# Kernel tuning notes

Hardware: AMD Instinct MI355X
Metric: run time of the kernel (lower is better)

The kernel has to match this reference:

```python
import jax, jax.numpy as jnp
import numpy as np

N = 50000        # nodes
E = 1_600_000    # edges (avg degree 32)
F_IN = 128       # node feature dim
H = 64           # hidden_channels
C = 19           # output classes
G = 512          # graphs in the batch


def setup_inputs() -> dict:
    key = jax.random.key(0)
    ks = jax.random.split(key, 9)
    x = jax.random.normal(ks[0], (N, F_IN), dtype=jnp.float32)
    edge_index = jax.random.randint(ks[1], (2, E), 0, N, dtype=jnp.int64)
    batch = jnp.sort(jax.random.randint(ks[2], (N,), 0, G, dtype=jnp.int64))
    W1 = jax.random.normal(ks[3], (F_IN, H), dtype=jnp.float32) / np.sqrt(F_IN)
    b1 = jnp.zeros((H,), dtype=jnp.float32)
    W2 = jax.random.normal(ks[4], (H, H), dtype=jnp.float32) / np.sqrt(H)
    b2 = jnp.zeros((H,), dtype=jnp.float32)
    W_out = jax.random.normal(ks[5], (H, C), dtype=jnp.float32) / np.sqrt(H)
    b_out = jnp.zeros((C,), dtype=jnp.float32)
    return {"x": x, "edge_index": edge_index, "batch": batch,
            "W1": W1, "b1": b1, "W2": W2, "b2": b2,
            "W_out": W_out, "b_out": b_out}


def _gcn_conv(x, src, dst, W, b, n_nodes):
    """PyG GCNConv: add self-loops, symmetric D^-1/2 (A+I) D^-1/2 norm,
    linear transform first, gather-scale-scatter aggregation, then bias."""
    x = x @ W  # [N, out]
    loop = jnp.arange(n_nodes, dtype=src.dtype)
    s = jnp.concatenate([src, loop])  # source (message origin)
    d = jnp.concatenate([dst, loop])  # target (aggregation site)
    deg = jax.ops.segment_sum(jnp.ones_like(d, dtype=x.dtype), d,
                              num_segments=n_nodes)
    dinv = jnp.where(deg > 0, jax.lax.rsqrt(deg), 0.0)
    norm = dinv[s] * dinv[d]                       # [E+N]
    msg = x[s] * norm[:, None]                     # gather + scale
    out = jax.ops.segment_sum(msg, d, num_segments=n_nodes)  # scatter-add
    return out + b


def reference(x, edge_index, batch, W1, b1, W2, b2, W_out, b_out):
    src, dst = edge_index[0], edge_index[1]
    h = _gcn_conv(x, src, dst, W1, b1, N)
    h = jax.nn.relu(h)
    # F.dropout(training=False) -> identity (eval mode)
    h = _gcn_conv(h, src, dst, W2, b2, N)
    # global mean pool over graphs
    sums = jax.ops.segment_sum(h, batch, num_segments=G)        # [G, H]
    cnts = jax.ops.segment_sum(jnp.ones((N,), h.dtype), batch,
                               num_segments=G)                  # [G]
    pooled = sums / jnp.maximum(cnts, 1.0)[:, None]
    return pooled @ W_out + b_out                               # [G, C]
```

## Files before the change

kernel.cpp:

```cpp
#include <hip/hip_runtime.h>
#include <hip/hip_bf16.h>

#define F_IN 128
#define HID  64
#define NCLS 19
#define BW   128
#define NBMAX 512
#define ACAP 3072
#define BCAP 8192
#define BKCAP 5120
#define W1STR 136
#define W2STR 72

typedef __bf16 bf16x8 __attribute__((ext_vector_type(8)));
typedef float  f32x4  __attribute__((ext_vector_type(4)));

__device__ __forceinline__ float ldf(const void* p, long i, int fp32) {
    if (fp32) return ((const float*)p)[i];
    return __bfloat162float(((const __hip_bfloat16*)p)[i]);
}
__device__ __forceinline__ int ldi(const void* p, long i, int i64) {
    if (i64) return (int)((const long long*)p)[i];
    return ((const int*)p)[i];
}
__device__ __forceinline__ unsigned short f2bf(float f) {
    __hip_bfloat16 h = __float2bfloat16(f);
    unsigned short r;
    __builtin_memcpy(&r, &h, 2);
    return r;
}
__device__ __forceinline__ float bflo(unsigned u) { return __uint_as_float(u << 16); }
__device__ __forceinline__ float bfhi(unsigned u) { return __uint_as_float(u & 0xffff0000u); }

__device__ __forceinline__ bf16x8 ldfrag(const unsigned short* p) {
    uint4 u = *(const uint4*)p;
    return __builtin_bit_cast(bf16x8, u);
}
__device__ __forceinline__ bf16x8 ldfrag_any(const void* p, long off, int fp32) {
    if (!fp32) return ldfrag((const unsigned short*)p + off);
    const float4* f = (const float4*)((const float*)p + off);
    float4 u0 = f[0];
    float4 u1 = f[1];
    uint4 u = make_uint4((unsigned)f2bf(u0.x) | ((unsigned)f2bf(u0.y) << 16),
                         (unsigned)f2bf(u0.z) | ((unsigned)f2bf(u0.w) << 16),
                         (unsigned)f2bf(u1.x) | ((unsigned)f2bf(u1.y) << 16),
                         (unsigned)f2bf(u1.z) | ((unsigned)f2bf(u1.w) << 16));
    return __builtin_bit_cast(bf16x8, u);
}

__global__ __launch_bounds__(512) void k_detect(const void* x, const void* ei, int* flags,
                                                int* __restrict__ bcur, int NB) {
    int t = threadIdx.x;
    for (int b = t; b < NB; b += 512) bcur[b] = b * BKCAP;
    if (t != 0) return;
    const unsigned* xw = (const unsigned*)x;
    int bf16 = 1;
    for (int i = 0; i < 16; ++i) {
        unsigned w = xw[i];
        int elo = (w >> 7) & 0xFF;
        int ehi = (w >> 23) & 0xFF;
        if (elo < 100 || elo > 140 || ehi < 100 || ehi > 140) bf16 = 0;
    }
    const unsigned* iw = (const unsigned*)ei;
    int i64 = 1; unsigned anyev = 0;
    for (int k = 0; k < 8; ++k) {
        if (iw[2 * k + 1] != 0) i64 = 0;
        anyev |= iw[2 * k];
    }
    if (anyev == 0) i64 = 0;
    flags[0] = bf16 ? 0 : 1;
    flags[1] = i64;
}

__global__ __launch_bounds__(256) void k_bounds(const void* __restrict__ batch, int N, int G,
                                                int* __restrict__ bounds,
                                                const int* __restrict__ flags) {
    int i64 = flags[1];
    int i = blockIdx.x * 256 + threadIdx.x;
    if (i >= N) return;
    int b = min(max(ldi(batch, i, i64), 0), G - 1);
    int p = (i == 0) ? -1 : min(max(ldi(batch, (long)i - 1, i64), 0), G - 1);
    for (int g = p + 1; g <= b; ++g) bounds[g] = i;
    if (i == N - 1)
        for (int g = b + 1; g <= G; ++g) bounds[g] = N;
}

__global__ __launch_bounds__(512) void k_sortA(const void* __restrict__ ei, int E, int nbuck,
                                               int* bcur, int* __restrict__ bkt,
                                               const int* __restrict__ flags) {
    __shared__ int lbuf[ACAP];
    __shared__ unsigned short lbkt[ACAP];
    __shared__ int lh[NBMAX];
    __shared__ int lsc[NBMAX];
    __shared__ int lcur[NBMAX];
    __shared__ int gbase[NBMAX];
    int i64 = flags[1];
    int t = threadIdx.x;
    int e0 = blockIdx.x * ACAP;
    int e1 = min(E, e0 + ACAP);
    int cnt = e1 - e0;
    lh[t] = 0;
    __syncthreads();
    for (int e = e0 + t; e < e1; e += 512)
        atomicAdd(&lh[(ldi(ei, (long)E + e, i64) >> 7) & (NBMAX - 1)], 1);
    __syncthreads();
    int v = lh[t];
    lsc[t] = v;
    __syncthreads();
    for (int off = 1; off < 512; off <<= 1) {
        int a = (t >= off) ? lsc[t - off] : 0;
        __syncthreads();
        lsc[t] += a;
        __syncthreads();
    }
    int ex = lsc[t] - v;
    lsc[t] = ex;
    lcur[t] = ex;
    gbase[t] = (v && t < nbuck) ? atomicAdd(&bcur[t], v) : 0;
    __syncthreads();
    for (int e = e0 + t; e < e1; e += 512) {
        int s = ldi(ei, e, i64);
        int d = ldi(ei, (long)E + e, i64);
        int b = (d >> 7) & (NBMAX - 1);
        int r = atomicAdd(&lcur[b], 1);
        r = min(max(r, 0), ACAP - 1);
        lbuf[r] = (s << 7) | (d & (BW - 1));
        lbkt[r] = (unsigned short)b;
    }
    __syncthreads();
    for (int i = t; i < cnt; i += 512) {
        int lo = lbkt[i];
        int idx = gbase[lo] + (i - lsc[lo]);
        if (idx >= lo * BKCAP && idx < (lo + 1) * BKCAP) bkt[idx] = lbuf[i];
    }
}

__global__ __launch_bounds__(256) void k_sortB(const int* __restrict__ bkt,
                                               const int* __restrict__ bcur,
                                               int N,
                                               int* __restrict__ csr,
                                               int* __restrict__ cursor,
                                               int* __restrict__ deg,
                                               float* __restrict__ dinv) {
    __shared__ int lcsr[BCAP];
    __shared__ int lh[BW], lsc[BW], lcur[BW];
    int b = blockIdx.x, t = threadIdx.x;
    int base = b * BKCAP;
    int cnt = min(max(bcur[b] - base, 0), BKCAP);
    int end = base + cnt;
    if (t < BW) lh[t] = 0;
    __syncthreads();
    for (int i = base + t; i < end; i += 256)
        atomicAdd(&lh[bkt[i] & (BW - 1)], 1);
    __syncthreads();
    if (t < BW) lsc[t] = lh[t];
    __syncthreads();
    for (int off = 1; off < BW; off <<= 1) {
        int a = (t < BW && t >= off) ? lsc[t - off] : 0;
        __syncthreads();
        if (t < BW) lsc[t] += a;
        __syncthreads();
    }
    if (t < BW) {
        int ex = lsc[t] - lh[t];
        lcur[t] = ex;
        int n = b * BW + t;
        if (n < N) {
            cursor[n] = base + ex;
            deg[n] = lh[t];
            dinv[n] = rsqrtf((float)(lh[t] + 1));
        }
    }
    __syncthreads();
    bool fits = (cnt <= BCAP);
    for (int i = base + t; i < end; i += 256) {
        int w = bkt[i];
        int r = atomicAdd(&lcur[w & (BW - 1)], 1);
        int sv = (int)((unsigned)w >> 7);
        if (sv >= N) sv = 0;
        if (fits) { r = min(max(r, 0), BCAP - 1); lcsr[r] = sv; }
        else { r = min(max(r, 0), BKCAP - 1); csr[base + r] = sv; }
    }
    __syncthreads();
    if (fits)
        for (int i = t; i < cnt; i += 256) csr[base + i] = lcsr[i];
}

__global__ __launch_bounds__(256) void k_gemm1(const void* __restrict__ x,
                                               const void* __restrict__ W,
                                               const float* __restrict__ dinv,
                                               unsigned short* __restrict__ t, int N,
                                               const int* __restrict__ flags) {
    __shared__ __align__(16) unsigned short wt[HID * W1STR];
    int fp32 = flags[0];
    int tid = threadIdx.x;
    if (fp32) {
        const float* wf = (const float*)W;
        for (int i = tid * 4; i < F_IN * HID; i += 1024) {
            float4 w4 = *(const float4*)(wf + i);
            int k = i >> 6, n = i & 63;
            wt[(n + 0) * W1STR + k] = f2bf(w4.x);
            wt[(n + 1) * W1STR + k] = f2bf(w4.y);
            wt[(n + 2) * W1STR + k] = f2bf(w4.z);
            wt[(n + 3) * W1STR + k] = f2bf(w4.w);
        }
    } else {
        for (int i = tid; i < F_IN * HID; i += 256) {
            int k = i >> 6, n = i & 63;
            wt[n * W1STR + k] = f2bf(ldf(W, i, 0));
        }
    }
    __syncthreads();
    int wv = tid >> 6, lane = tid & 63;
    int quad = lane >> 4, l16 = lane & 15;
    int r0 = blockIdx.x * 64 + wv * 16;
    int rowA = min(r0 + l16, N - 1);
    bf16x8 a[4];
#pragma unroll
    for (int kq = 0; kq < 4; ++kq)
        a[kq] = ldfrag_any(x, (long)rowA * F_IN + kq * 32 + quad * 8, fp32);
    float di[4];
    int rowC = r0 + quad * 4;
#pragma unroll
    for (int r = 0; r < 4; ++r) di[r] = (rowC + r < N) ? dinv[rowC + r] : 0.f;
#pragma unroll
    for (int cg = 0; cg < 4; ++cg) {
        int col = cg * 16 + l16;
        f32x4 acc = {0.f, 0.f, 0.f, 0.f};
#pragma unroll
        for (int kq = 0; kq < 4; ++kq) {
            bf16x8 b = ldfrag(wt + col * W1STR + kq * 32 + quad * 8);
            acc = __builtin_amdgcn_mfma_f32_16x16x32_bf16(a[kq], b, acc, 0, 0, 0);
        }
#pragma unroll
        for (int r = 0; r < 4; ++r) {
            int row = rowC + r;
            if (row < N) t[(size_t)row * HID + col] = f2bf(di[r] * acc[r]);
        }
    }
}

__global__ __launch_bounds__(256) void k_gemm2(const unsigned short* __restrict__ h,
                                               const void* __restrict__ W,
                                               const float* __restrict__ dinv,
                                               unsigned short* __restrict__ t, int N,
                                               const int* __restrict__ flags) {
    __shared__ __align__(16) unsigned short wt[HID * W2STR];
    int fp32 = flags[0];
    int tid = threadIdx.x;
    if (fp32) {
        const float* wf = (const float*)W;
        for (int i = tid * 4; i < HID * HID; i += 1024) {
            float4 w4 = *(const float4*)(wf + i);
            int k = i >> 6, n = i & 63;
            wt[(n + 0) * W2STR + k] = f2bf(w4.x);
            wt[(n + 1) * W2STR + k] = f2bf(w4.y);
            wt[(n + 2) * W2STR + k] = f2bf(w4.z);
            wt[(n + 3) * W2STR + k] = f2bf(w4.w);
        }
    } else {
        for (int i = tid; i < HID * HID; i += 256) {
            int k = i >> 6, n = i & 63;
            wt[n * W2STR + k] = f2bf(ldf(W, i, 0));
        }
    }
    __syncthreads();
    int wv = tid >> 6, lane = tid & 63;
    int quad = lane >> 4, l16 = lane & 15;
    int r0 = blockIdx.x * 64 + wv * 16;
    int rowA = min(r0 + l16, N - 1);
    bf16x8 a[2];
#pragma unroll
    for (int kq = 0; kq < 2; ++kq)
        a[kq] = ldfrag(h + (size_t)rowA * HID + kq * 32 + quad * 8);
    float di[4];
    int rowC = r0 + quad * 4;
#pragma unroll
    for (int r = 0; r < 4; ++r) di[r] = (rowC + r < N) ? dinv[rowC + r] : 0.f;
#pragma unroll
    for (int cg = 0; cg < 4; ++cg) {
        int col = cg * 16 + l16;
        f32x4 acc = {0.f, 0.f, 0.f, 0.f};
#pragma unroll
        for (int kq = 0; kq < 2; ++kq) {
            bf16x8 b = ldfrag(wt + col * W2STR + kq * 32 + quad * 8);
            acc = __builtin_amdgcn_mfma_f32_16x16x32_bf16(a[kq], b, acc, 0, 0, 0);
        }
#pragma unroll
        for (int r = 0; r < 4; ++r) {
            int row = rowC + r;
            if (row < N) t[(size_t)row * HID + col] = f2bf(di[r] * acc[r]);
        }
    }
}

template <bool RELU>
__global__ __launch_bounds__(256) void k_agg(const unsigned short* __restrict__ t,
                                             const int* __restrict__ csr,
                                             const int* __restrict__ cursor,
                                             const int* __restrict__ deg,
                                             const float* __restrict__ dinv,
                                             const void* __restrict__ bias,
                                             unsigned short* __restrict__ out,
                                             int N, int SZ, const int* __restrict__ flags) {
    __shared__ float sbias[HID];
    __shared__ int scur[8];
    __shared__ int sdeg[8];
    __shared__ float sdv[8];
    int tid = threadIdx.x;
    int nb = blockIdx.x * 8;
    if (tid < HID) sbias[tid] = ldf(bias, tid, flags[0]);
    if (tid >= 64 && tid < 72) {
        int q = tid - 64;
        int node = nb + q;
        int c = 0, d = 0;
        float dv = 0.f;
        if (node < N) { c = cursor[node]; d = deg[node]; dv = dinv[node]; }
        scur[q] = c; sdeg[q] = d; sdv[q] = dv;
    }
    __syncthreads();
    int wv = tid >> 6, lane = tid & 63;
    int half = lane >> 5;
    int idx = wv * 2 + half;
    int node = nb + idx;
    int l = lane & 31;
    int g = l >> 3;
    int l8 = (l & 7) * 8;
    bool alive = (node < N);
    int snode = alive ? node : 0;
    int beg = scur[idx];
    int dg = sdeg[idx];
    beg = min(max(beg, 0), SZ);
    int end = beg + min(max(dg, 0), SZ - beg);
    uint4 sv = make_uint4(0u, 0u, 0u, 0u);
    if (g == 0) sv = *(const uint4*)(t + (size_t)snode * HID + l8);
    float a0 = 0.f, a1 = 0.f, a2 = 0.f, a3 = 0.f;
    float a4 = 0.f, a5 = 0.f, a6 = 0.f, a7 = 0.f;
    for (int e = beg; e < end; e += 32) {
        int s[8];
#pragma unroll
        for (int k = 0; k < 8; ++k) {
            int i = e + 4 * k + g;
            int si = csr[i < end ? i : end - 1];
            s[k] = ((unsigned)si < (unsigned)N) ? si : 0;
        }
        uint4 v[8];
#pragma unroll
        for (int k = 0; k < 8; ++k)
            v[k] = *(const uint4*)(t + (size_t)s[k] * HID + l8);
#pragma unroll
        for (int k = 0; k < 8; ++k) {
            if (e + 4 * k + g < end) {
                a0 += bflo(v[k].x); a1 += bfhi(v[k].x);
                a2 += bflo(v[k].y); a3 += bfhi(v[k].y);
                a4 += bflo(v[k].z); a5 += bfhi(v[k].z);
                a6 += bflo(v[k].w); a7 += bfhi(v[k].w);
            }
        }
    }
#pragma unroll
    for (int m = 8; m <= 16; m <<= 1) {
        a0 += __shfl_xor(a0, m); a1 += __shfl_xor(a1, m);
        a2 += __shfl_xor(a2, m); a3 += __shfl_xor(a3, m);
        a4 += __shfl_xor(a4, m); a5 += __shfl_xor(a5, m);
        a6 += __shfl_xor(a6, m); a7 += __shfl_xor(a7, m);
    }
    if (g == 0 && alive) {
        a0 += bflo(sv.x); a1 += bfhi(sv.x); a2 += bflo(sv.y); a3 += bfhi(sv.y);
        a4 += bflo(sv.z); a5 += bfhi(sv.z); a6 += bflo(sv.w); a7 += bfhi(sv.w);
        float di = sdv[idx];
        float v0 = di * a0 + sbias[l8 + 0];
        float v1 = di * a1 + sbias[l8 + 1];
        float v2 = di * a2 + sbias[l8 + 2];
        float v3 = di * a3 + sbias[l8 + 3];
        float v4 = di * a4 + sbias[l8 + 4];
        float v5 = di * a5 + sbias[l8 + 5];
        float v6 = di * a6 + sbias[l8 + 6];
        float v7 = di * a7 + sbias[l8 + 7];
        if (RELU) {
            v0 = fmaxf(v0, 0.f); v1 = fmaxf(v1, 0.f); v2 = fmaxf(v2, 0.f); v3 = fmaxf(v3, 0.f);
            v4 = fmaxf(v4, 0.f); v5 = fmaxf(v5, 0.f); v6 = fmaxf(v6, 0.f); v7 = fmaxf(v7, 0.f);
        }
        uint4 pk;
        pk.x = (unsigned)f2bf(v0) | ((unsigned)f2bf(v1) << 16);
        pk.y = (unsigned)f2bf(v2) | ((unsigned)f2bf(v3) << 16);
        pk.z = (unsigned)f2bf(v4) | ((unsigned)f2bf(v5) << 16);
        pk.w = (unsigned)f2bf(v6) | ((unsigned)f2bf(v7) << 16);
        *(uint4*)(out + (size_t)node * HID + l8) = pk;
    }
}

__global__ __launch_bounds__(256) void k_poolout(const unsigned short* __restrict__ h2,
                                                 const int* __restrict__ bounds, int N,
                                                 const void* __restrict__ Wout,
                                                 const void* __restrict__ bout,
                                                 void* __restrict__ out,
                                                 const int* __restrict__ flags) {
    __shared__ float pr[HID];
    __shared__ float sacc[4][HID];
    int g = blockIdx.x;
    int start = min(max(bounds[g], 0), N);
    int endg = min(max(bounds[g + 1], start), N);
    int tid = threadIdx.x;
    int wv = tid >> 6, lane = tid & 63;
    int half = lane >> 5;
    int l = lane & 31;
    float s0 = 0.f, s1 = 0.f;
    for (int r = start + wv * 2 + half; r < endg; r += 8) {
        unsigned u = *(const unsigned*)(h2 + (size_t)r * HID + 2 * l);
        s0 += bflo(u);
        s1 += bfhi(u);
    }
    s0 += __shfl_xor(s0, 32);
    s1 += __shfl_xor(s1, 32);
    if (lane < 32) {
        sacc[wv][2 * l] = s0;
        sacc[wv][2 * l + 1] = s1;
    }
    __syncthreads();
    if (tid < HID) {
        float inv = 1.f / fmaxf((float)(endg - start), 1.f);
        pr[tid] = (sacc[0][tid] + sacc[1][tid] + sacc[2][tid] + sacc[3][tid]) * inv;
    }
    __syncthreads();
    int fp32 = flags[0];
    if (tid < NCLS) {
        float acc = ldf(bout, tid, fp32);
#pragma unroll 4
        for (int k = 0; k < HID; ++k)
            acc += pr[k] * ldf(Wout, k * NCLS + tid, fp32);
        if (fp32) ((float*)out)[g * NCLS + tid] = acc;
        else ((__hip_bfloat16*)out)[g * NCLS + tid] = __float2bfloat16(acc);
    }
}

extern "C" void kernel_launch(void* const* d_in, const int* in_sizes, int n_in,
                              void* d_out, int out_size, void* d_ws, size_t ws_size,
                              hipStream_t stream) {
    const void* x    = d_in[0];
    const void* ei   = d_in[1];
    const void* bat  = d_in[2];
    const void* W1   = d_in[3];
    const void* b1   = d_in[4];
    const void* W2   = d_in[5];
    const void* b2   = d_in[6];
    const void* Wout = d_in[7];
    const void* bout = d_in[8];

    const int N = in_sizes[0] / F_IN;
    const int E = in_sizes[1] / 2;
    const int G = out_size / NCLS;
    const int NB = (N + BW - 1) / BW;
    const int SZ = NB * BKCAP;

    char* ws = (char*)d_ws;
    size_t off = 0;
    auto carve = [&](size_t bytes) -> void* {
        void* p = ws + off;
        off = (off + bytes + 255) & ~(size_t)255;
        return p;
    };
    int*            flags  = (int*)carve(64);
    int*            deg    = (int*)carve((size_t)N * 4);
    int*            cursor = (int*)carve((size_t)N * 4);
    float*          dinv   = (float*)carve((size_t)N * 4);
    int*            bcur   = (int*)carve((size_t)NB * 4);
    int*            bounds = (int*)carve((size_t)(G + 1) * 4);
    int*            csr    = (int*)carve((size_t)SZ * 4);
    int*            bkt    = (int*)carve((size_t)SZ * 4);
    unsigned short* t      = (unsigned short*)carve((size_t)N * HID * 2);
    unsigned short* h      = (unsigned short*)carve((size_t)N * HID * 2);
    (void)ws_size; (void)n_in;

    k_detect<<<1, 512, 0, stream>>>(x, ei, flags, bcur, NB);
    k_bounds<<<(N + 255) / 256, 256, 0, stream>>>(bat, N, G, bounds, flags);

    int na = (E + ACAP - 1) / ACAP;
    k_sortA<<<na, 512, 0, stream>>>(ei, E, NB, bcur, bkt, flags);
    k_sortB<<<NB, 256, 0, stream>>>(bkt, bcur, N, csr, cursor, deg, dinv);

    int gb = (N + 63) / 64;
    int ab = (N + 7) / 8;
    k_gemm1<<<gb, 256, 0, stream>>>(x, W1, dinv, t, N, flags);
    k_agg<true><<<ab, 256, 0, stream>>>(t, csr, cursor, deg, dinv, b1, h, N, SZ, flags);
    k_gemm2<<<gb, 256, 0, stream>>>(h, W2, dinv, t, N, flags);
    k_agg<false><<<ab, 256, 0, stream>>>(t, csr, cursor, deg, dinv, b2, h, N, SZ, flags);
    k_poolout<<<G, 256, 0, stream>>>(h, bounds, N, Wout, bout, d_out, flags);
}
```

Baseline: 205.7 us.

## Speed up sort prefix scans, stage buckets in LDS, and split aggregation tail

The 512-entry block scan in k_sortA becomes a wavefront shuffle scan plus a small cross-wave fixup, which removes many barriers. k_sortB now runs with 512 threads and reads each bucket from global memory once into LDS, reusing that copy for the histogram and the scatter pass. The shared buffer is sized to the bucket capacity, so the global-memory fallback is gone. The aggregation loop gets a full-chunk fast path with no bounds checks and uses nontemporal loads for CSR indices, keeping a guarded tail iteration for the remainder.

```diff
diff --git a/kernel.cpp b/kernel.cpp
--- a/kernel.cpp
+++ b/kernel.cpp
@@ -7,7 +7,6 @@
 #define BW   128
 #define NBMAX 512
 #define ACAP 3072
-#define BCAP 8192
 #define BKCAP 5120
 #define W1STR 136
 #define W2STR 72
@@ -94,6 +93,7 @@
     __shared__ int lsc[NBMAX];
     __shared__ int lcur[NBMAX];
     __shared__ int gbase[NBMAX];
+    __shared__ int wpart[8];
     int i64 = flags[1];
     int t = threadIdx.x;
     int e0 = blockIdx.x * ACAP;
@@ -105,15 +105,22 @@
         atomicAdd(&lh[(ldi(ei, (long)E + e, i64) >> 7) & (NBMAX - 1)], 1);
     __syncthreads();
     int v = lh[t];
-    lsc[t] = v;
-    __syncthreads();
-    for (int off = 1; off < 512; off <<= 1) {
-        int a = (t >= off) ? lsc[t - off] : 0;
-        __syncthreads();
-        lsc[t] += a;
-        __syncthreads();
-    }
-    int ex = lsc[t] - v;
+    int lane = t & 63, wq = t >> 6;
+    int incl = v;
+#pragma unroll
+    for (int off = 1; off < 64; off <<= 1) {
+        int n = __shfl_up(incl, off);
+        if (lane >= off) incl += n;
+    }
+    if (lane == 63) wpart[wq] = incl;
+    __syncthreads();
+    if (t == 0) {
+        int acc = 0;
+#pragma unroll
+        for (int i = 0; i < 8; ++i) { int xx = wpart[i]; wpart[i] = acc; acc += xx; }
+    }
+    __syncthreads();
+    int ex = wpart[wq] + incl - v;
     lsc[t] = ex;
     lcur[t] = ex;
     gbase[t] = (v && t < nbuck) ? atomicAdd(&bcur[t], v) : 0;
@@ -135,23 +142,26 @@
     }
 }
 
-__global__ __launch_bounds__(256) void k_sortB(const int* __restrict__ bkt,
+__global__ __launch_bounds__(512) void k_sortB(const int* __restrict__ bkt,
                                                const int* __restrict__ bcur,
                                                int N,
                                                int* __restrict__ csr,
                                                int* __restrict__ cursor,
                                                int* __restrict__ deg,
                                                float* __restrict__ dinv) {
-    __shared__ int lcsr[BCAP];
+    __shared__ int lstage[BKCAP];
+    __shared__ int lcsr[BKCAP];
     __shared__ int lh[BW], lsc[BW], lcur[BW];
     int b = blockIdx.x, t = threadIdx.x;
     int base = b * BKCAP;
     int cnt = min(max(bcur[b] - base, 0), BKCAP);
-    int end = base + cnt;
     if (t < BW) lh[t] = 0;
     __syncthreads();
-    for (int i = base + t; i < end; i += 256)
-        atomicAdd(&lh[bkt[i] & (BW - 1)], 1);
+    for (int i = t; i < cnt; i += 512) {
+        int w = __builtin_nontemporal_load(&bkt[base + i]);
+        lstage[i] = w;
+        atomicAdd(&lh[w & (BW - 1)], 1);
+    }
     __syncthreads();
     if (t < BW) lsc[t] = lh[t];
     __syncthreads();
@@ -172,18 +182,16 @@
         }
     }
     __syncthreads();
-    bool fits = (cnt <= BCAP);
-    for (int i = base + t; i < end; i += 256) {
-        int w = bkt[i];
+    for (int i = t; i < cnt; i += 512) {
+        int w = lstage[i];
         int r = atomicAdd(&lcur[w & (BW - 1)], 1);
         int sv = (int)((unsigned)w >> 7);
         if (sv >= N) sv = 0;
-        if (fits) { r = min(max(r, 0), BCAP - 1); lcsr[r] = sv; }
-        else { r = min(max(r, 0), BKCAP - 1); csr[base + r] = sv; }
-    }
-    __syncthreads();
-    if (fits)
-        for (int i = t; i < cnt; i += 256) csr[base + i] = lcsr[i];
+        r = min(max(r, 0), BKCAP - 1);
+        lcsr[r] = sv;
+    }
+    __syncthreads();
+    for (int i = t; i < cnt; i += 512) csr[base + i] = lcsr[i];
 }
 
 __global__ __launch_bounds__(256) void k_gemm1(const void* __restrict__ x,
@@ -336,12 +344,32 @@
     if (g == 0) sv = *(const uint4*)(t + (size_t)snode * HID + l8);
     float a0 = 0.f, a1 = 0.f, a2 = 0.f, a3 = 0.f;
     float a4 = 0.f, a5 = 0.f, a6 = 0.f, a7 = 0.f;
-    for (int e = beg; e < end; e += 32) {
+    int e = beg;
+    for (; e + 32 <= end; e += 32) {
+        int s[8];
+#pragma unroll
+        for (int k = 0; k < 8; ++k) {
+            int si = __builtin_nontemporal_load(&csr[e + 4 * k + g]);
+            s[k] = ((unsigned)si < (unsigned)N) ? si : 0;
+        }
+        uint4 v[8];
+#pragma unroll
+        for (int k = 0; k < 8; ++k)
+            v[k] = *(const uint4*)(t + (size_t)s[k] * HID + l8);
+#pragma unroll
+        for (int k = 0; k < 8; ++k) {
+            a0 += bflo(v[k].x); a1 += bfhi(v[k].x);
+            a2 += bflo(v[k].y); a3 += bfhi(v[k].y);
+            a4 += bflo(v[k].z); a5 += bfhi(v[k].z);
+            a6 += bflo(v[k].w); a7 += bfhi(v[k].w);
+        }
+    }
+    if (e < end) {
         int s[8];
 #pragma unroll
         for (int k = 0; k < 8; ++k) {
             int i = e + 4 * k + g;
-            int si = csr[i < end ? i : end - 1];
+            int si = __builtin_nontemporal_load(&csr[i < end ? i : end - 1]);
             s[k] = ((unsigned)si < (unsigned)N) ? si : 0;
         }
         uint4 v[8];
@@ -477,7 +505,7 @@
 
     int na = (E + ACAP - 1) / ACAP;
     k_sortA<<<na, 512, 0, stream>>>(ei, E, NB, bcur, bkt, flags);
-    k_sortB<<<NB, 256, 0, stream>>>(bkt, bcur, N, csr, cursor, deg, dinv);
+    k_sortB<<<NB, 512, 0, stream>>>(bkt, bcur, N, csr, cursor, deg, dinv);
 
     int gb = (N + 63) / 64;
     int ab = (N + 7) / 8;
```

Result: no change. 204.9 us (-0.4%).
